# Performance work log

Hardware: AMD Instinct MI355X
Metric: run time of the kernel (lower is better)

## Reference

```python
import jax, jax.numpy as jnp
import numpy as np

DIM = 192
HEADS = 6
EMB4 = 192  # embed_dim * 4

def layer_norm(x, g, b, eps=1e-5):
    mu = jnp.mean(x, axis=-1, keepdims=True)
    var = jnp.var(x, axis=-1, keepdims=True)
    return (x - mu) * jax.lax.rsqrt(var + eps) * g + b

def setup_inputs() -> dict:
    key = jax.random.key(0)
    ks = jax.random.split(key, 8)
    B, C, H, W = 4, DIM, 128, 128
    M = 256
    s = lambda fan: 1.0 / np.sqrt(fan)
    return {
        "x": jax.random.normal(ks[0], (B, C, H, W), jnp.float32),
        "prior": jax.random.normal(ks[1], (B, M, EMB4), jnp.float32),
        "ln1_g": jnp.ones((DIM,), jnp.float32),
        "ln1_b": jnp.zeros((DIM,), jnp.float32),
        "ln2_g": jnp.ones((EMB4,), jnp.float32),
        "ln2_b": jnp.zeros((EMB4,), jnp.float32),
        "Wq": jax.random.normal(ks[2], (DIM, DIM), jnp.float32) * s(DIM),
        "Wkv": jax.random.normal(ks[3], (EMB4, 2 * DIM), jnp.float32) * s(EMB4),
        "Wp": jax.random.normal(ks[4], (DIM, DIM), jnp.float32) * s(DIM),
        "bp": jnp.zeros((DIM,), jnp.float32),
    }

def reference(x, prior, ln1_g, ln1_b, ln2_g, ln2_b, Wq, Wkv, Wp, bp):
    B, C, H, W = x.shape
    nh = HEADS
    hd = C // nh
    scale = hd ** (-0.5)
    xt = x.reshape(B, C, H * W).transpose(0, 2, 1)  # b n c
    _x = layer_norm(xt, ln1_g, ln1_b)
    pr = layer_norm(prior, ln2_g, ln2_b)
    q = _x @ Wq                      # b n (h d)
    kv = pr @ Wkv                    # b m (2 h d)
    k, v = jnp.split(kv, 2, axis=-1)
    N = H * W
    Mlen = prior.shape[1]
    q = q.reshape(B, N, nh, hd).transpose(0, 2, 1, 3)      # b h n d
    k = k.reshape(B, Mlen, nh, hd).transpose(0, 2, 1, 3)   # b h m d
    v = v.reshape(B, Mlen, nh, hd).transpose(0, 2, 1, 3)   # b h m d
    attn = jnp.einsum('bhnd,bhmd->bhnm', q, k) * scale
    attn = jax.nn.softmax(attn, axis=-1)
    out = jnp.einsum('bhnm,bhmd->bhnd', attn, v)
    out = out.transpose(0, 2, 1, 3).reshape(B, N, C)
    out = out @ Wp + bp
    y = xt + out
    return y.transpose(0, 2, 1).reshape(B, C, H, W)
```

## Files before the change

### kernel.cpp

```cpp
#include <hip/hip_runtime.h>

typedef unsigned short u16;
typedef unsigned int u32;

#define C_DIM 192
#define N_TOK 16384
#define M_LEN 256
#define HD 32
#define NH 6

#define AF_STRIDE 3080

typedef __attribute__((ext_vector_type(8))) short short8v;
typedef __attribute__((ext_vector_type(4))) float float4v;

__device__ __forceinline__ u32 cvt_pk_bf16(float lo, float hi) {
    u32 r;
    asm("v_cvt_pk_bf16_f32 %0, %1, %2" : "=v"(r) : "v"(lo), "v"(hi));
    return r;
}
__device__ __forceinline__ u16 f2bf_hw(float f) {
    return (u16)cvt_pk_bf16(f, f);
}

__global__ __launch_bounds__(256) void wq_prep(
    const float* __restrict__ Wq, u16* __restrict__ WqF)
{
    int gt = blockIdx.x * 256 + threadIdx.x;
    int f = gt >> 6, lane = gt & 63;
    int q8 = lane >> 4, ln = lane & 15;
    int wv = f / 18, r = f % 18;
    int kt = r / 3, jj = r % 3;
    const float* w0 = Wq + (kt * 32 + q8 * 8) * C_DIM + (wv * 3 + jj) * 16 + ln;
    union { u32 w[4]; short8v v; } out;
#pragma unroll
    for (int j = 0; j < 4; ++j)
        out.w[j] = cvt_pk_bf16(w0[(2 * j) * C_DIM], w0[(2 * j + 1) * C_DIM]);
    *(short8v*)&WqF[f * 512 + lane * 8] = out.v;
}

__global__ __launch_bounds__(256) void ln1_q_mfma(
    const float* __restrict__ x, const float* __restrict__ g,
    const float* __restrict__ beta, const u16* __restrict__ WqF,
    u16* __restrict__ q)
{
    __shared__ u16 Af[4 * AF_STRIDE];
    __shared__ u16 Tq[64 * 200];
    __shared__ float part[64][4][2];
    __shared__ float mu_s[64], rs_s[64];
    int b = blockIdx.x >> 8;
    int n0 = (blockIdx.x & 255) * 64;
    int t = threadIdx.x;
    int wv = t >> 6, lane = t & 63;

    float xv[48];
    {
        const float* xb = x + (((size_t)(b * C_DIM + wv * 48)) << 14) + n0 + lane;
        float s1 = 0.f, s2 = 0.f;
#pragma unroll
        for (int i = 0; i < 48; ++i) {
            float f = xb[(size_t)i << 14];
            xv[i] = f; s1 += f; s2 += f * f;
        }
        part[lane][wv][0] = s1; part[lane][wv][1] = s2;
    }
    __syncthreads();
    if (t < 64) {
        float a  = part[t][0][0] + part[t][1][0] + part[t][2][0] + part[t][3][0];
        float c2 = part[t][0][1] + part[t][1][1] + part[t][2][1] + part[t][3][1];
        float mu = a * (1.f / C_DIM);
        mu_s[t] = mu;
        rs_s[t] = rsqrtf(c2 * (1.f / C_DIM) - mu * mu + 1e-5f);
    }
    __syncthreads();

    {
        float mu = mu_s[lane], rs = rs_s[lane];
        int mt2 = lane >> 4, ln2 = lane & 15;
        u32* A32 = (u32*)Af;
#pragma unroll
        for (int i = 0; i < 48; i += 2) {
            int c = wv * 48 + i;
            float f0 = (xv[i]     - mu) * rs * g[c]     + beta[c];
            float f1 = (xv[i + 1] - mu) * rs * g[c + 1] + beta[c + 1];
            int kt = c >> 5, k8 = (c & 31) >> 3, j = c & 7;
            A32[(mt2 * AF_STRIDE + kt * 512 + k8 * 128 + ln2 * 8 + j) >> 1] =
                cvt_pk_bf16(f0, f1);
        }
    }
    __syncthreads();

    int q8 = lane >> 4, ln = lane & 15;
    short8v Bf[18];
#pragma unroll
    for (int i = 0; i < 18; ++i)
        Bf[i] = *(const short8v*)&WqF[(wv * 18 + i) * 512 + lane * 8];

#pragma unroll
    for (int mt = 0; mt < 4; ++mt) {
        float4v acc[3] = {{0.f,0.f,0.f,0.f},{0.f,0.f,0.f,0.f},{0.f,0.f,0.f,0.f}};
#pragma unroll
        for (int kt = 0; kt < 6; ++kt) {
            short8v a = *(const short8v*)&Af[mt * AF_STRIDE + kt * 512 + lane * 8];
#pragma unroll
            for (int jj = 0; jj < 3; ++jj)
                acc[jj] = __builtin_amdgcn_mfma_f32_16x16x32_bf16(a, Bf[kt * 3 + jj], acc[jj], 0, 0, 0);
        }
#pragma unroll
        for (int jj = 0; jj < 3; ++jj)
#pragma unroll
            for (int r = 0; r < 4; ++r)
                Tq[(mt * 16 + q8 * 4 + r) * 200 + (wv * 3 + jj) * 16 + ln] = f2bf_hw(acc[jj][r]);
    }
    __syncthreads();

    {
        int tok = t >> 2, pp = t & 3;
        const uint4* src = (const uint4*)&Tq[tok * 200 + pp * 48];
        uint4* dst = (uint4*)(q + ((size_t)(b * N_TOK + n0 + tok)) * C_DIM + pp * 48);
#pragma unroll
        for (int i = 0; i < 6; ++i) dst[i] = src[i];
    }
}

__global__ __launch_bounds__(192) void ln2_kv_kernel(
    const float* __restrict__ prior, const float* __restrict__ g,
    const float* __restrict__ beta, const float* __restrict__ Wkv,
    float* __restrict__ k, float* __restrict__ v)
{
    __shared__ float pr[C_DIM];
    __shared__ float red[3][2];
    int row = blockIdx.x;
    int tid = threadIdx.x;
    int wv = tid >> 6;
    float val = prior[row * C_DIM + tid];
    float s1 = val, s2 = val * val;
#pragma unroll
    for (int m = 1; m < 64; m <<= 1) {
        s1 += __shfl_xor(s1, m);
        s2 += __shfl_xor(s2, m);
    }
    if ((tid & 63) == 0) { red[wv][0] = s1; red[wv][1] = s2; }
    __syncthreads();
    float a  = red[0][0] + red[1][0] + red[2][0];
    float c2 = red[0][1] + red[1][1] + red[2][1];
    float mu = a * (1.f / C_DIM);
    float rs = rsqrtf(c2 * (1.f / C_DIM) - mu * mu + 1e-5f);
    pr[tid] = (val - mu) * rs * g[tid] + beta[tid];
    __syncthreads();
    float ka = 0.f, va = 0.f;
    for (int c = 0; c < C_DIM; ++c) {
        float p = pr[c];
        ka += p * Wkv[c * 384 + tid];
        va += p * Wkv[c * 384 + 192 + tid];
    }
    k[row * C_DIM + tid] = ka;
    v[row * C_DIM + tid] = va;
}

__global__ __launch_bounds__(256) void kv_prep(
    const float* __restrict__ kg, const float* __restrict__ vg,
    u16* __restrict__ KfG, u16* __restrict__ VfG)
{
    int bh = blockIdx.x;
    int h = bh % NH, b = bh / NH;
    int tid = threadIdx.x;
    const float scale = 0.17677669529663687f;
    u16* Kd = KfG + bh * 8192;
    u16* Vd = VfG + bh * 8192;
    for (int i = tid; i < 8192; i += 256) {
        int key = i >> 5, dim = i & 31;
        int gidx = (b * M_LEN + key) * C_DIM + h * HD + dim;
        {
            float f = kg[gidx] * scale;
            int kt = key >> 4, r = key & 15, qd = dim >> 3, j = dim & 7;
            Kd[kt * 512 + (qd * 16 + r) * 8 + j] = f2bf_hw(f);
        }
        {
            float f = vg[gidx];
            int kt = key >> 4, r = key & 15;
            int qd = r >> 2, reg = r & 3;
            int P = kt >> 1;
            int j = reg + 4 * (kt & 1);
            int dh = dim >> 4, n = dim & 15;
            Vd[(P * 2 + dh) * 512 + (qd * 16 + n) * 8 + j] = f2bf_hw(f);
        }
    }
}

__global__ __launch_bounds__(256) void attn_mfma_kernel(
    const u16* __restrict__ q, const u16* __restrict__ KfG,
    const u16* __restrict__ VfG, u16* __restrict__ att)
{
    __shared__ u16 sh[16384];
    int tb = blockIdx.x & 63;
    int bh = blockIdx.x >> 6;
    int h = bh % NH, b = bh / NH;
    int tid = threadIdx.x;
    int wave = tid >> 6, lane = tid & 63;
    int quad = lane >> 4, ln = lane & 15;

    const u16* qbase = q + ((size_t)(b * N_TOK + tb * 256 + wave * 16 + ln)) * C_DIM
                         + h * HD + quad * 8;
    short8v qnext = *(const short8v*)qbase;

    {
        const uint4* Ks = (const uint4*)(KfG + bh * 8192);
        const uint4* Vs = (const uint4*)(VfG + bh * 8192);
        uint4* d = (uint4*)sh;
#pragma unroll
        for (int i = tid; i < 2048; i += 256)
            d[i] = (i < 1024) ? Ks[i] : Vs[i - 1024];
    }
    __syncthreads();

    const u16* Kf = sh;
    const u16* Vf = sh + 8192;
    const float LOG2E = 1.4426950408889634f;

    for (int rep = 0; rep < 4; ++rep) {
        short8v qf = qnext;
        int nrep = rep < 3 ? rep + 1 : 3;
        qnext = *(const short8v*)(qbase + (size_t)nrep * 64 * C_DIM);

        float4v s[16];
#pragma unroll
        for (int kt = 0; kt < 16; ++kt) {
            short8v kf = *(const short8v*)&Kf[kt * 512 + lane * 8];
            float4v z = {0.f, 0.f, 0.f, 0.f};
            s[kt] = __builtin_amdgcn_mfma_f32_16x16x32_bf16(kf, qf, z, 0, 0, 0);
        }

        float mx = fmaxf(fmaxf(s[0][0], s[0][1]), fmaxf(s[0][2], s[0][3]));
#pragma unroll
        for (int kt = 1; kt < 16; ++kt)
            mx = fmaxf(fmaxf(mx, s[kt][0]),
                       fmaxf(s[kt][1], fmaxf(s[kt][2], s[kt][3])));
        mx = fmaxf(mx, __shfl_xor(mx, 16));
        mx = fmaxf(mx, __shfl_xor(mx, 32));

        float nm = -mx * LOG2E;
        float l = 0.f;
#pragma unroll
        for (int kt = 0; kt < 16; ++kt) {
#pragma unroll
            for (int r = 0; r < 4; ++r) {
                float p = __builtin_amdgcn_exp2f(fmaf(s[kt][r], LOG2E, nm));
                s[kt][r] = p;
                l += p;
            }
        }
        l += __shfl_xor(l, 16);
        l += __shfl_xor(l, 32);
        float inv = __builtin_amdgcn_rcpf(l);

        float4v o0 = {0.f, 0.f, 0.f, 0.f}, o1 = {0.f, 0.f, 0.f, 0.f};
#pragma unroll
        for (int P = 0; P < 8; ++P) {
            union { u32 w[4]; short8v v; } pf;
            pf.w[0] = cvt_pk_bf16(s[2 * P][0],     s[2 * P][1]);
            pf.w[1] = cvt_pk_bf16(s[2 * P][2],     s[2 * P][3]);
            pf.w[2] = cvt_pk_bf16(s[2 * P + 1][0], s[2 * P + 1][1]);
            pf.w[3] = cvt_pk_bf16(s[2 * P + 1][2], s[2 * P + 1][3]);
            short8v v0 = *(const short8v*)&Vf[(P * 2 + 0) * 512 + lane * 8];
            short8v v1 = *(const short8v*)&Vf[(P * 2 + 1) * 512 + lane * 8];
            o0 = __builtin_amdgcn_mfma_f32_16x16x32_bf16(pf.v, v0, o0, 0, 0, 0);
            o1 = __builtin_amdgcn_mfma_f32_16x16x32_bf16(pf.v, v1, o1, 0, 0, 0);
        }

        int token0 = tb * 256 + rep * 64 + wave * 16;
#pragma unroll
        for (int r = 0; r < 4; ++r) {
            float invr = __shfl(inv, quad * 4 + r);
            u16* row = att + ((size_t)(b * N_TOK + token0 + quad * 4 + r)) * C_DIM + h * HD;
            row[ln]      = f2bf_hw(o0[r] * invr);
            row[16 + ln] = f2bf_hw(o1[r] * invr);
        }
    }
}

__global__ __launch_bounds__(256) void proj_res_mfma(
    const u16* __restrict__ att, const float* __restrict__ Wp,
    const u16* __restrict__ WpF, const float* __restrict__ bp,
    const float* __restrict__ x, float* __restrict__ y)
{
    __shared__ float Tf[C_DIM * 68];
    int b = blockIdx.x >> 8;
    int n0 = (blockIdx.x & 255) * 64;
    int t = threadIdx.x;
    int wv = t >> 6, lane = t & 63;
    int q8 = lane >> 4, ln = lane & 15;

    short8v Bf[18];
    if (WpF) {
#pragma unroll
        for (int i = 0; i < 18; ++i)
            Bf[i] = *(const short8v*)&WpF[(wv * 18 + i) * 512 + lane * 8];
    } else {
#pragma unroll
        for (int kt = 0; kt < 6; ++kt) {
#pragma unroll
            for (int jj = 0; jj < 3; ++jj) {
                const float* w0 = Wp + (kt * 32 + q8 * 8) * C_DIM + (wv * 3 + jj) * 16 + ln;
                union { u32 w[4]; short8v v; } f;
#pragma unroll
                for (int wj = 0; wj < 4; ++wj)
                    f.w[wj] = cvt_pk_bf16(w0[(2 * wj) * C_DIM], w0[(2 * wj + 1) * C_DIM]);
                Bf[kt * 3 + jj] = f.v;
            }
        }
    }

#pragma unroll
    for (int mt = 0; mt < 4; ++mt) {
        const u16* ab = att + ((size_t)(b * N_TOK + n0 + mt * 16 + ln)) * C_DIM + q8 * 8;
        float4v acc[3] = {{0.f,0.f,0.f,0.f},{0.f,0.f,0.f,0.f},{0.f,0.f,0.f,0.f}};
#pragma unroll
        for (int kt = 0; kt < 6; ++kt) {
            short8v a = *(const short8v*)(ab + kt * 32);
#pragma unroll
            for (int jj = 0; jj < 3; ++jj)
                acc[jj] = __builtin_amdgcn_mfma_f32_16x16x32_bf16(a, Bf[kt * 3 + jj], acc[jj], 0, 0, 0);
        }
#pragma unroll
        for (int jj = 0; jj < 3; ++jj)
#pragma unroll
            for (int r = 0; r < 4; ++r)
                Tf[((wv * 3 + jj) * 16 + ln) * 68 + mt * 16 + q8 * 4 + r] = acc[jj][r];
    }
    __syncthreads();

    {
        int r0 = t >> 4;
        int p  = t & 15;
#pragma unroll
        for (int pass = 0; pass < 12; ++pass) {
            int c = pass * 16 + r0;
            float bias = bp[c];
            float4 a = *(const float4*)&Tf[c * 68 + p * 4];
            const float4* xr = (const float4*)(x + (((size_t)(b * C_DIM + c)) << 14) + n0);
            float4*       yr = (float4*)(y + (((size_t)(b * C_DIM + c)) << 14) + n0);
            float4 u = xr[p];
            float4 w;
            w.x = a.x + bias + u.x;
            w.y = a.y + bias + u.y;
            w.z = a.z + bias + u.z;
            w.w = a.w + bias + u.w;
            yr[p] = w;
        }
    }
}

extern "C" void kernel_launch(void* const* d_in, const int* in_sizes, int n_in,
                              void* d_out, int out_size, void* d_ws, size_t ws_size,
                              hipStream_t stream) {
    const float* x     = (const float*)d_in[0];
    const float* prior = (const float*)d_in[1];
    const float* ln1_g = (const float*)d_in[2];
    const float* ln1_b = (const float*)d_in[3];
    const float* ln2_g = (const float*)d_in[4];
    const float* ln2_b = (const float*)d_in[5];
    const float* Wq    = (const float*)d_in[6];
    const float* Wkv   = (const float*)d_in[7];
    const float* Wp    = (const float*)d_in[8];
    const float* bp    = (const float*)d_in[9];

    char* outc = (char*)d_out;
    u16*   q    = (u16*)outc;
    float* kbuf = (float*)(outc + 25165824);
    float* vbuf = (float*)(outc + 25952256);
    u16*   WqF  = (u16*)(outc + 26738688);
    u16*   KfG  = (u16*)(outc + 26812416);
    u16*   VfG  = (u16*)(outc + 27205632);
    u16*   att  = (u16*)d_ws;
    float* y    = (float*)d_out;

    bool has_wpf = ws_size >= (size_t)25165824 + 73728;
    u16* WpF = has_wpf ? (u16*)((char*)d_ws + 25165824) : (u16*)nullptr;

    wq_prep<<<18, 256, 0, stream>>>(Wq, WqF);
    if (has_wpf) wq_prep<<<18, 256, 0, stream>>>(Wp, WpF);
    ln1_q_mfma<<<1024, 256, 0, stream>>>(x, ln1_g, ln1_b, WqF, q);
    ln2_kv_kernel<<<1024, 192, 0, stream>>>(prior, ln2_g, ln2_b, Wkv, kbuf, vbuf);
    kv_prep<<<24, 256, 0, stream>>>(kbuf, vbuf, KfG, VfG);
    attn_mfma_kernel<<<1536, 256, 0, stream>>>(q, KfG, VfG, att);
    proj_res_mfma<<<1024, 256, 0, stream>>>(att, Wp, WpF, bp, x, y);
}
```

Baseline: 204.5 us.

## Fuse attention with output projection and fold KV fragment prep into LN2

Attention and the output projection now run in one kernel per 64-token tile. The kernel loops over all 6 heads, keeps the bf16 attention output in LDS and feeds it straight into the Wp MFMA, so the attention tensor never makes a global round trip. The LN2/KV kernel writes scaled bf16 MFMA fragments directly, which removes the fp32 k/v buffers and the kv_prep launch, and the two weight-prep launches are merged into one. In exchange, K/V are read straight from global/L2 inside the head loop instead of being staged in LDS, and the fused path only runs when the workspace is large enough.

After: 241.2 us. 17.9% more time.

```diff
diff --git a/kernel.cpp b/kernel.cpp
--- a/kernel.cpp
+++ b/kernel.cpp
@@ -23,20 +23,24 @@
     return (u16)cvt_pk_bf16(f, f);
 }
 
-__global__ __launch_bounds__(256) void wq_prep(
-    const float* __restrict__ Wq, u16* __restrict__ WqF)
+__global__ __launch_bounds__(256) void w_prep2(
+    const float* __restrict__ Wq, u16* __restrict__ WqF,
+    const float* __restrict__ Wp, u16* __restrict__ WpF)
 {
-    int gt = blockIdx.x * 256 + threadIdx.x;
+    int bb = blockIdx.x;
+    const float* W = (bb < 18) ? Wq : Wp;
+    u16* outp = (bb < 18) ? WqF : WpF;
+    int gt = (bb % 18) * 256 + threadIdx.x;
     int f = gt >> 6, lane = gt & 63;
     int q8 = lane >> 4, ln = lane & 15;
     int wv = f / 18, r = f % 18;
     int kt = r / 3, jj = r % 3;
-    const float* w0 = Wq + (kt * 32 + q8 * 8) * C_DIM + (wv * 3 + jj) * 16 + ln;
+    const float* w0 = W + (kt * 32 + q8 * 8) * C_DIM + (wv * 3 + jj) * 16 + ln;
     union { u32 w[4]; short8v v; } out;
 #pragma unroll
     for (int j = 0; j < 4; ++j)
         out.w[j] = cvt_pk_bf16(w0[(2 * j) * C_DIM], w0[(2 * j + 1) * C_DIM]);
-    *(short8v*)&WqF[f * 512 + lane * 8] = out.v;
+    *(short8v*)&outp[f * 512 + lane * 8] = out.v;
 }
 
 __global__ __launch_bounds__(256) void ln1_q_mfma(
@@ -123,10 +127,10 @@
     }
 }
 
-__global__ __launch_bounds__(192) void ln2_kv_kernel(
+__global__ __launch_bounds__(192) void ln2_kv_frag(
     const float* __restrict__ prior, const float* __restrict__ g,
     const float* __restrict__ beta, const float* __restrict__ Wkv,
-    float* __restrict__ k, float* __restrict__ v)
+    u16* __restrict__ KfG, u16* __restrict__ VfG)
 {
     __shared__ float pr[C_DIM];
     __shared__ float red[3][2];
@@ -154,180 +158,137 @@
         ka += p * Wkv[c * 384 + tid];
         va += p * Wkv[c * 384 + 192 + tid];
     }
-    k[row * C_DIM + tid] = ka;
-    v[row * C_DIM + tid] = va;
-}
-
-__global__ __launch_bounds__(256) void kv_prep(
-    const float* __restrict__ kg, const float* __restrict__ vg,
-    u16* __restrict__ KfG, u16* __restrict__ VfG)
-{
-    int bh = blockIdx.x;
-    int h = bh % NH, b = bh / NH;
-    int tid = threadIdx.x;
-    const float scale = 0.17677669529663687f;
-    u16* Kd = KfG + bh * 8192;
-    u16* Vd = VfG + bh * 8192;
-    for (int i = tid; i < 8192; i += 256) {
-        int key = i >> 5, dim = i & 31;
-        int gidx = (b * M_LEN + key) * C_DIM + h * HD + dim;
-        {
-            float f = kg[gidx] * scale;
-            int kt = key >> 4, r = key & 15, qd = dim >> 3, j = dim & 7;
-            Kd[kt * 512 + (qd * 16 + r) * 8 + j] = f2bf_hw(f);
-        }
-        {
-            float f = vg[gidx];
-            int kt = key >> 4, r = key & 15;
-            int qd = r >> 2, reg = r & 3;
-            int P = kt >> 1;
-            int j = reg + 4 * (kt & 1);
-            int dh = dim >> 4, n = dim & 15;
-            Vd[(P * 2 + dh) * 512 + (qd * 16 + n) * 8 + j] = f2bf_hw(f);
-        }
-    }
-}
-
-__global__ __launch_bounds__(256) void attn_mfma_kernel(
+    int b = row >> 8, m = row & 255;
+    int h = tid >> 5, dim = tid & 31;
+    int bh = b * NH + h;
+    int kt = m >> 4, r = m & 15;
+    {
+        int qd = dim >> 3, j = dim & 7;
+        KfG[bh * 8192 + kt * 512 + (qd * 16 + r) * 8 + j] =
+            f2bf_hw(ka * 0.17677669529663687f);
+    }
+    {
+        int qd = r >> 2, reg = r & 3;
+        int P = kt >> 1;
+        int j = reg + 4 * (kt & 1);
+        int dh = dim >> 4, n = dim & 15;
+        VfG[bh * 8192 + (P * 2 + dh) * 512 + (qd * 16 + n) * 8 + j] = f2bf_hw(va);
+    }
+}
+
+__global__ __launch_bounds__(256) void attn_proj_fused(
     const u16* __restrict__ q, const u16* __restrict__ KfG,
-    const u16* __restrict__ VfG, u16* __restrict__ att)
-{
-    __shared__ u16 sh[16384];
-    int tb = blockIdx.x & 63;
-    int bh = blockIdx.x >> 6;
-    int h = bh % NH, b = bh / NH;
-    int tid = threadIdx.x;
-    int wave = tid >> 6, lane = tid & 63;
-    int quad = lane >> 4, ln = lane & 15;
-
-    const u16* qbase = q + ((size_t)(b * N_TOK + tb * 256 + wave * 16 + ln)) * C_DIM
-                         + h * HD + quad * 8;
-    short8v qnext = *(const short8v*)qbase;
-
-    {
-        const uint4* Ks = (const uint4*)(KfG + bh * 8192);
-        const uint4* Vs = (const uint4*)(VfG + bh * 8192);
-        uint4* d = (uint4*)sh;
-#pragma unroll
-        for (int i = tid; i < 2048; i += 256)
-            d[i] = (i < 1024) ? Ks[i] : Vs[i - 1024];
-    }
-    __syncthreads();
-
-    const u16* Kf = sh;
-    const u16* Vf = sh + 8192;
-    const float LOG2E = 1.4426950408889634f;
-
-    for (int rep = 0; rep < 4; ++rep) {
-        short8v qf = qnext;
-        int nrep = rep < 3 ? rep + 1 : 3;
-        qnext = *(const short8v*)(qbase + (size_t)nrep * 64 * C_DIM);
-
-        float4v s[16];
-#pragma unroll
-        for (int kt = 0; kt < 16; ++kt) {
-            short8v kf = *(const short8v*)&Kf[kt * 512 + lane * 8];
-            float4v z = {0.f, 0.f, 0.f, 0.f};
-            s[kt] = __builtin_amdgcn_mfma_f32_16x16x32_bf16(kf, qf, z, 0, 0, 0);
-        }
-
-        float mx = fmaxf(fmaxf(s[0][0], s[0][1]), fmaxf(s[0][2], s[0][3]));
-#pragma unroll
-        for (int kt = 1; kt < 16; ++kt)
-            mx = fmaxf(fmaxf(mx, s[kt][0]),
-                       fmaxf(s[kt][1], fmaxf(s[kt][2], s[kt][3])));
-        mx = fmaxf(mx, __shfl_xor(mx, 16));
-        mx = fmaxf(mx, __shfl_xor(mx, 32));
-
-        float nm = -mx * LOG2E;
-        float l = 0.f;
-#pragma unroll
-        for (int kt = 0; kt < 16; ++kt) {
-#pragma unroll
-            for (int r = 0; r < 4; ++r) {
-                float p = __builtin_amdgcn_exp2f(fmaf(s[kt][r], LOG2E, nm));
-                s[kt][r] = p;
-                l += p;
-            }
-        }
-        l += __shfl_xor(l, 16);
-        l += __shfl_xor(l, 32);
-        float inv = __builtin_amdgcn_rcpf(l);
-
-        float4v o0 = {0.f, 0.f, 0.f, 0.f}, o1 = {0.f, 0.f, 0.f, 0.f};
-#pragma unroll
-        for (int P = 0; P < 8; ++P) {
-            union { u32 w[4]; short8v v; } pf;
-            pf.w[0] = cvt_pk_bf16(s[2 * P][0],     s[2 * P][1]);
-            pf.w[1] = cvt_pk_bf16(s[2 * P][2],     s[2 * P][3]);
-            pf.w[2] = cvt_pk_bf16(s[2 * P + 1][0], s[2 * P + 1][1]);
-            pf.w[3] = cvt_pk_bf16(s[2 * P + 1][2], s[2 * P + 1][3]);
-            short8v v0 = *(const short8v*)&Vf[(P * 2 + 0) * 512 + lane * 8];
-            short8v v1 = *(const short8v*)&Vf[(P * 2 + 1) * 512 + lane * 8];
-            o0 = __builtin_amdgcn_mfma_f32_16x16x32_bf16(pf.v, v0, o0, 0, 0, 0);
-            o1 = __builtin_amdgcn_mfma_f32_16x16x32_bf16(pf.v, v1, o1, 0, 0, 0);
-        }
-
-        int token0 = tb * 256 + rep * 64 + wave * 16;
-#pragma unroll
-        for (int r = 0; r < 4; ++r) {
-            float invr = __shfl(inv, quad * 4 + r);
-            u16* row = att + ((size_t)(b * N_TOK + token0 + quad * 4 + r)) * C_DIM + h * HD;
-            row[ln]      = f2bf_hw(o0[r] * invr);
-            row[16 + ln] = f2bf_hw(o1[r] * invr);
-        }
-    }
-}
-
-__global__ __launch_bounds__(256) void proj_res_mfma(
-    const u16* __restrict__ att, const float* __restrict__ Wp,
-    const u16* __restrict__ WpF, const float* __restrict__ bp,
-    const float* __restrict__ x, float* __restrict__ y)
+    const u16* __restrict__ VfG, const u16* __restrict__ WpF,
+    const float* __restrict__ bp, const float* __restrict__ x,
+    float* __restrict__ y)
 {
     __shared__ float Tf[C_DIM * 68];
-    int b = blockIdx.x >> 8;
+    u16* att_lds = (u16*)Tf;
+    int b  = blockIdx.x >> 8;
     int n0 = (blockIdx.x & 255) * 64;
     int t = threadIdx.x;
-    int wv = t >> 6, lane = t & 63;
-    int q8 = lane >> 4, ln = lane & 15;
+    int wave = t >> 6, lane = t & 63;
+    int quad = lane >> 4, ln = lane & 15;
+    const float LOG2E = 1.4426950408889634f;
+
+    {
+        const u16* qrow = q + ((size_t)(b * N_TOK + n0 + wave * 16 + ln)) * C_DIM + quad * 8;
+        const u16* Kbase = KfG + b * NH * 8192;
+        const u16* Vbase = VfG + b * NH * 8192;
+        short8v qnext = *(const short8v*)qrow;
+        for (int h = 0; h < NH; ++h) {
+            short8v qf = qnext;
+            int hn = (h < NH - 1) ? h + 1 : h;
+            qnext = *(const short8v*)(qrow + hn * HD);
+            const u16* Kf = Kbase + h * 8192;
+            const u16* Vf = Vbase + h * 8192;
+
+            float4v s[16];
+#pragma unroll
+            for (int kt = 0; kt < 16; ++kt) {
+                short8v kf = *(const short8v*)&Kf[kt * 512 + lane * 8];
+                float4v z = {0.f, 0.f, 0.f, 0.f};
+                s[kt] = __builtin_amdgcn_mfma_f32_16x16x32_bf16(kf, qf, z, 0, 0, 0);
+            }
+
+            float mx = fmaxf(fmaxf(s[0][0], s[0][1]), fmaxf(s[0][2], s[0][3]));
+#pragma unroll
+            for (int kt = 1; kt < 16; ++kt)
+                mx = fmaxf(fmaxf(mx, s[kt][0]),
+                           fmaxf(s[kt][1], fmaxf(s[kt][2], s[kt][3])));
+            mx = fmaxf(mx, __shfl_xor(mx, 16));
+            mx = fmaxf(mx, __shfl_xor(mx, 32));
+
+            float nm = -mx * LOG2E;
+            float l = 0.f;
+#pragma unroll
+            for (int kt = 0; kt < 16; ++kt) {
+#pragma unroll
+                for (int r = 0; r < 4; ++r) {
+                    float p = __builtin_amdgcn_exp2f(fmaf(s[kt][r], LOG2E, nm));
+                    s[kt][r] = p;
+                    l += p;
+                }
+            }
+            l += __shfl_xor(l, 16);
+            l += __shfl_xor(l, 32);
+            float inv = __builtin_amdgcn_rcpf(l);
+
+            float4v o0 = {0.f, 0.f, 0.f, 0.f}, o1 = {0.f, 0.f, 0.f, 0.f};
+#pragma unroll
+            for (int P = 0; P < 8; ++P) {
+                union { u32 w[4]; short8v v; } pf;
+                pf.w[0] = cvt_pk_bf16(s[2 * P][0],     s[2 * P][1]);
+                pf.w[1] = cvt_pk_bf16(s[2 * P][2],     s[2 * P][3]);
+                pf.w[2] = cvt_pk_bf16(s[2 * P + 1][0], s[2 * P + 1][1]);
+                pf.w[3] = cvt_pk_bf16(s[2 * P + 1][2], s[2 * P + 1][3]);
+                short8v v0 = *(const short8v*)&Vf[(P * 2 + 0) * 512 + lane * 8];
+                short8v v1 = *(const short8v*)&Vf[(P * 2 + 1) * 512 + lane * 8];
+                o0 = __builtin_amdgcn_mfma_f32_16x16x32_bf16(pf.v, v0, o0, 0, 0, 0);
+                o1 = __builtin_amdgcn_mfma_f32_16x16x32_bf16(pf.v, v1, o1, 0, 0, 0);
+            }
+
+#pragma unroll
+            for (int r = 0; r < 4; ++r) {
+                float invr = __shfl(inv, quad * 4 + r);
+                u16* rw = &att_lds[(wave * 16 + quad * 4 + r) * 200 + h * HD];
+                rw[ln]      = f2bf_hw(o0[r] * invr);
+                rw[16 + ln] = f2bf_hw(o1[r] * invr);
+            }
+        }
+    }
+    __syncthreads();
 
     short8v Bf[18];
-    if (WpF) {
-#pragma unroll
-        for (int i = 0; i < 18; ++i)
-            Bf[i] = *(const short8v*)&WpF[(wv * 18 + i) * 512 + lane * 8];
-    } else {
+#pragma unroll
+    for (int i = 0; i < 18; ++i)
+        Bf[i] = *(const short8v*)&WpF[(wave * 18 + i) * 512 + lane * 8];
+
+    float4v acc[4][3];
+#pragma unroll
+    for (int mt = 0; mt < 4; ++mt) {
+#pragma unroll
+        for (int jj = 0; jj < 3; ++jj) {
+            float4v z = {0.f, 0.f, 0.f, 0.f};
+            acc[mt][jj] = z;
+        }
 #pragma unroll
         for (int kt = 0; kt < 6; ++kt) {
-#pragma unroll
-            for (int jj = 0; jj < 3; ++jj) {
-                const float* w0 = Wp + (kt * 32 + q8 * 8) * C_DIM + (wv * 3 + jj) * 16 + ln;
-                union { u32 w[4]; short8v v; } f;
-#pragma unroll
-                for (int wj = 0; wj < 4; ++wj)
-                    f.w[wj] = cvt_pk_bf16(w0[(2 * wj) * C_DIM], w0[(2 * wj + 1) * C_DIM]);
-                Bf[kt * 3 + jj] = f.v;
-            }
-        }
-    }
-
-#pragma unroll
-    for (int mt = 0; mt < 4; ++mt) {
-        const u16* ab = att + ((size_t)(b * N_TOK + n0 + mt * 16 + ln)) * C_DIM + q8 * 8;
-        float4v acc[3] = {{0.f,0.f,0.f,0.f},{0.f,0.f,0.f,0.f},{0.f,0.f,0.f,0.f}};
-#pragma unroll
-        for (int kt = 0; kt < 6; ++kt) {
-            short8v a = *(const short8v*)(ab + kt * 32);
+            short8v a = *(const short8v*)&att_lds[(mt * 16 + ln) * 200 + quad * 8 + kt * 32];
 #pragma unroll
             for (int jj = 0; jj < 3; ++jj)
-                acc[jj] = __builtin_amdgcn_mfma_f32_16x16x32_bf16(a, Bf[kt * 3 + jj], acc[jj], 0, 0, 0);
-        }
+                acc[mt][jj] = __builtin_amdgcn_mfma_f32_16x16x32_bf16(a, Bf[kt * 3 + jj], acc[mt][jj], 0, 0, 0);
+        }
+    }
+    __syncthreads();
+
+#pragma unroll
+    for (int mt = 0; mt < 4; ++mt)
 #pragma unroll
         for (int jj = 0; jj < 3; ++jj)
 #pragma unroll
             for (int r = 0; r < 4; ++r)
-                Tf[((wv * 3 + jj) * 16 + ln) * 68 + mt * 16 + q8 * 4 + r] = acc[jj][r];
-    }
+                Tf[((wave * 3 + jj) * 16 + ln) * 68 + mt * 16 + quad * 4 + r] = acc[mt][jj][r];
     __syncthreads();
 
     {
@@ -351,6 +312,169 @@
     }
 }
 
+__global__ __launch_bounds__(256) void attn_mfma_kernel(
+    const u16* __restrict__ q, const u16* __restrict__ KfG,
+    const u16* __restrict__ VfG, u16* __restrict__ att)
+{
+    __shared__ u16 sh[16384];
+    int tb = blockIdx.x & 63;
+    int bh = blockIdx.x >> 6;
+    int h = bh % NH, b = bh / NH;
+    int tid = threadIdx.x;
+    int wave = tid >> 6, lane = tid & 63;
+    int quad = lane >> 4, ln = lane & 15;
+
+    const u16* qbase = q + ((size_t)(b * N_TOK + tb * 256 + wave * 16 + ln)) * C_DIM
+                         + h * HD + quad * 8;
+    short8v qnext = *(const short8v*)qbase;
+
+    {
+        const uint4* Ks = (const uint4*)(KfG + bh * 8192);
+        const uint4* Vs = (const uint4*)(VfG + bh * 8192);
+        uint4* d = (uint4*)sh;
+#pragma unroll
+        for (int i = tid; i < 2048; i += 256)
+            d[i] = (i < 1024) ? Ks[i] : Vs[i - 1024];
+    }
+    __syncthreads();
+
+    const u16* Kf = sh;
+    const u16* Vf = sh + 8192;
+    const float LOG2E = 1.4426950408889634f;
+
+    for (int rep = 0; rep < 4; ++rep) {
+        short8v qf = qnext;
+        int nrep = rep < 3 ? rep + 1 : 3;
+        qnext = *(const short8v*)(qbase + (size_t)nrep * 64 * C_DIM);
+
+        float4v s[16];
+#pragma unroll
+        for (int kt = 0; kt < 16; ++kt) {
+            short8v kf = *(const short8v*)&Kf[kt * 512 + lane * 8];
+            float4v z = {0.f, 0.f, 0.f, 0.f};
+            s[kt] = __builtin_amdgcn_mfma_f32_16x16x32_bf16(kf, qf, z, 0, 0, 0);
+        }
+
+        float mx = fmaxf(fmaxf(s[0][0], s[0][1]), fmaxf(s[0][2], s[0][3]));
+#pragma unroll
+        for (int kt = 1; kt < 16; ++kt)
+            mx = fmaxf(fmaxf(mx, s[kt][0]),
+                       fmaxf(s[kt][1], fmaxf(s[kt][2], s[kt][3])));
+        mx = fmaxf(mx, __shfl_xor(mx, 16));
+        mx = fmaxf(mx, __shfl_xor(mx, 32));
+
+        float nm = -mx * LOG2E;
+        float l = 0.f;
+#pragma unroll
+        for (int kt = 0; kt < 16; ++kt) {
+#pragma unroll
+            for (int r = 0; r < 4; ++r) {
+                float p = __builtin_amdgcn_exp2f(fmaf(s[kt][r], LOG2E, nm));
+                s[kt][r] = p;
+                l += p;
+            }
+        }
+        l += __shfl_xor(l, 16);
+        l += __shfl_xor(l, 32);
+        float inv = __builtin_amdgcn_rcpf(l);
+
+        float4v o0 = {0.f, 0.f, 0.f, 0.f}, o1 = {0.f, 0.f, 0.f, 0.f};
+#pragma unroll
+        for (int P = 0; P < 8; ++P) {
+            union { u32 w[4]; short8v v; } pf;
+            pf.w[0] = cvt_pk_bf16(s[2 * P][0],     s[2 * P][1]);
+            pf.w[1] = cvt_pk_bf16(s[2 * P][2],     s[2 * P][3]);
+            pf.w[2] = cvt_pk_bf16(s[2 * P + 1][0], s[2 * P + 1][1]);
+            pf.w[3] = cvt_pk_bf16(s[2 * P + 1][2], s[2 * P + 1][3]);
+            short8v v0 = *(const short8v*)&Vf[(P * 2 + 0) * 512 + lane * 8];
+            short8v v1 = *(const short8v*)&Vf[(P * 2 + 1) * 512 + lane * 8];
+            o0 = __builtin_amdgcn_mfma_f32_16x16x32_bf16(pf.v, v0, o0, 0, 0, 0);
+            o1 = __builtin_amdgcn_mfma_f32_16x16x32_bf16(pf.v, v1, o1, 0, 0, 0);
+        }
+
+        int token0 = tb * 256 + rep * 64 + wave * 16;
+#pragma unroll
+        for (int r = 0; r < 4; ++r) {
+            float invr = __shfl(inv, quad * 4 + r);
+            u16* row = att + ((size_t)(b * N_TOK + token0 + quad * 4 + r)) * C_DIM + h * HD;
+            row[ln]      = f2bf_hw(o0[r] * invr);
+            row[16 + ln] = f2bf_hw(o1[r] * invr);
+        }
+    }
+}
+
+__global__ __launch_bounds__(256) void proj_res_mfma(
+    const u16* __restrict__ att, const float* __restrict__ Wp,
+    const u16* __restrict__ WpF, const float* __restrict__ bp,
+    const float* __restrict__ x, float* __restrict__ y)
+{
+    __shared__ float Tf[C_DIM * 68];
+    int b = blockIdx.x >> 8;
+    int n0 = (blockIdx.x & 255) * 64;
+    int t = threadIdx.x;
+    int wv = t >> 6, lane = t & 63;
+    int q8 = lane >> 4, ln = lane & 15;
+
+    short8v Bf[18];
+    if (WpF) {
+#pragma unroll
+        for (int i = 0; i < 18; ++i)
+            Bf[i] = *(const short8v*)&WpF[(wv * 18 + i) * 512 + lane * 8];
+    } else {
+#pragma unroll
+        for (int kt = 0; kt < 6; ++kt) {
+#pragma unroll
+            for (int jj = 0; jj < 3; ++jj) {
+                const float* w0 = Wp + (kt * 32 + q8 * 8) * C_DIM + (wv * 3 + jj) * 16 + ln;
+                union { u32 w[4]; short8v v; } f;
+#pragma unroll
+                for (int wj = 0; wj < 4; ++wj)
+                    f.w[wj] = cvt_pk_bf16(w0[(2 * wj) * C_DIM], w0[(2 * wj + 1) * C_DIM]);
+                Bf[kt * 3 + jj] = f.v;
+            }
+        }
+    }
+
+#pragma unroll
+    for (int mt = 0; mt < 4; ++mt) {
+        const u16* ab = att + ((size_t)(b * N_TOK + n0 + mt * 16 + ln)) * C_DIM + q8 * 8;
+        float4v acc[3] = {{0.f,0.f,0.f,0.f},{0.f,0.f,0.f,0.f},{0.f,0.f,0.f,0.f}};
+#pragma unroll
+        for (int kt = 0; kt < 6; ++kt) {
+            short8v a = *(const short8v*)(ab + kt * 32);
+#pragma unroll
+            for (int jj = 0; jj < 3; ++jj)
+                acc[jj] = __builtin_amdgcn_mfma_f32_16x16x32_bf16(a, Bf[kt * 3 + jj], acc[jj], 0, 0, 0);
+        }
+#pragma unroll
+        for (int jj = 0; jj < 3; ++jj)
+#pragma unroll
+            for (int r = 0; r < 4; ++r)
+                Tf[((wv * 3 + jj) * 16 + ln) * 68 + mt * 16 + q8 * 4 + r] = acc[jj][r];
+    }
+    __syncthreads();
+
+    {
+        int r0 = t >> 4;
+        int p  = t & 15;
+#pragma unroll
+        for (int pass = 0; pass < 12; ++pass) {
+            int c = pass * 16 + r0;
+            float bias = bp[c];
+            float4 a = *(const float4*)&Tf[c * 68 + p * 4];
+            const float4* xr = (const float4*)(x + (((size_t)(b * C_DIM + c)) << 14) + n0);
+            float4*       yr = (float4*)(y + (((size_t)(b * C_DIM + c)) << 14) + n0);
+            float4 u = xr[p];
+            float4 w;
+            w.x = a.x + bias + u.x;
+            w.y = a.y + bias + u.y;
+            w.z = a.z + bias + u.z;
+            w.w = a.w + bias + u.w;
+            yr[p] = w;
+        }
+    }
+}
+
 extern "C" void kernel_launch(void* const* d_in, const int* in_sizes, int n_in,
                               void* d_out, int out_size, void* d_ws, size_t ws_size,
                               hipStream_t stream) {
@@ -366,23 +490,34 @@
     const float* bp    = (const float*)d_in[9];
 
     char* outc = (char*)d_out;
-    u16*   q    = (u16*)outc;
-    float* kbuf = (float*)(outc + 25165824);
-    float* vbuf = (float*)(outc + 25952256);
-    u16*   WqF  = (u16*)(outc + 26738688);
-    u16*   KfG  = (u16*)(outc + 26812416);
-    u16*   VfG  = (u16*)(outc + 27205632);
-    u16*   att  = (u16*)d_ws;
-    float* y    = (float*)d_out;
-
-    bool has_wpf = ws_size >= (size_t)25165824 + 73728;
-    u16* WpF = has_wpf ? (u16*)((char*)d_ws + 25165824) : (u16*)nullptr;
-
-    wq_prep<<<18, 256, 0, stream>>>(Wq, WqF);
-    if (has_wpf) wq_prep<<<18, 256, 0, stream>>>(Wp, WpF);
-    ln1_q_mfma<<<1024, 256, 0, stream>>>(x, ln1_g, ln1_b, WqF, q);
-    ln2_kv_kernel<<<1024, 192, 0, stream>>>(prior, ln2_g, ln2_b, Wkv, kbuf, vbuf);
-    kv_prep<<<24, 256, 0, stream>>>(kbuf, vbuf, KfG, VfG);
-    attn_mfma_kernel<<<1536, 256, 0, stream>>>(q, KfG, VfG, att);
-    proj_res_mfma<<<1024, 256, 0, stream>>>(att, Wp, WpF, bp, x, y);
-}
+    float* y = (float*)d_out;
+
+    const size_t needF = 25165824ull + 393216ull + 393216ull + 73728ull;
+    if (ws_size >= needF) {
+        char* wsc = (char*)d_ws;
+        u16* qb  = (u16*)wsc;
+        u16* KfG = (u16*)(wsc + 25165824);
+        u16* VfG = (u16*)(wsc + 25165824 + 393216);
+        u16* WpF = (u16*)(wsc + 25165824 + 786432);
+        u16* WqF = (u16*)outc;
+
+        w_prep2<<<36, 256, 0, stream>>>(Wq, WqF, Wp, WpF);
+        ln1_q_mfma<<<1024, 256, 0, stream>>>(x, ln1_g, ln1_b, WqF, qb);
+        ln2_kv_frag<<<1024, 192, 0, stream>>>(prior, ln2_g, ln2_b, Wkv, KfG, VfG);
+        attn_proj_fused<<<1024, 256, 0, stream>>>(qb, KfG, VfG, WpF, bp, x, y);
+    } else {
+        u16*   qb   = (u16*)outc;
+        u16*   WqF  = (u16*)(outc + 26738688);
+        u16*   KfG  = (u16*)(outc + 26812416);
+        u16*   VfG  = (u16*)(outc + 27205632);
+        u16*   att  = (u16*)d_ws;
+        bool has_wpf = ws_size >= 25165824ull + 73728ull;
+        u16* WpF = has_wpf ? (u16*)((char*)d_ws + 25165824) : (u16*)nullptr;
+
+        w_prep2<<<has_wpf ? 36 : 18, 256, 0, stream>>>(Wq, WqF, Wp, has_wpf ? WpF : WqF);
+        ln1_q_mfma<<<1024, 256, 0, stream>>>(x, ln1_g, ln1_b, WqF, qb);
+        ln2_kv_frag<<<1024, 192, 0, stream>>>(prior, ln2_g, ln2_b, Wkv, KfG, VfG);
+        attn_mfma_kernel<<<1536, 256, 0, stream>>>(qb, KfG, VfG, att);
+        proj_res_mfma<<<1024, 256, 0, stream>>>(att, Wp, WpF, bp, x, y);
+    }
+}
```
